# Performance work log

Measured on AMD Instinct MI355X. Metric: run time of the kernel, lower is better.

## Reference

```python
import jax, jax.numpy as jnp
import numpy as np


def setup_inputs() -> dict:
    key = jax.random.key(0)
    k1, k2 = jax.random.split(key)
    # NCHW input activations
    x = jax.random.normal(k1, (32, 256, 56, 56), dtype=jnp.float32)
    # OIHW weight; centered small-uniform so sign() is +/-1 with equal probability
    # (torch init is rand()*0.001, all-positive, which would make sign degenerate
    #  for kernel testing; magnitude scale kept comparable)
    weight = (jax.random.uniform(k2, (256, 256, 3, 3), dtype=jnp.float32) - 0.5) * 0.002
    return {"x": x, "weight": weight}


def reference(x, weight):
    # per-output-channel scaling factor: mean |w| over (in, kh, kw), detached
    scale = jax.lax.stop_gradient(
        jnp.mean(jnp.abs(weight), axis=(1, 2, 3), keepdims=True)
    )  # [O,1,1,1]
    w_clip = jnp.clip(weight, -1.0, 1.0)
    # STE: forward value = scale * sign(w); gradient flows through clip(w)
    binary_w = jax.lax.stop_gradient(scale * jnp.sign(weight) - w_clip) + w_clip
    y = jax.lax.conv_general_dilated(
        x,
        binary_w,
        window_strides=(1, 1),
        padding=((1, 1), (1, 1)),
        dimension_numbers=("NCHW", "OIHW", "NCHW"),
        feature_group_count=1,
    )
    return y
```

## Files before the change

### kernel.cpp

```cpp
#include <hip/hip_runtime.h>
#include <stdint.h>

typedef __attribute__((ext_vector_type(8))) short bf16x8;
typedef __attribute__((ext_vector_type(16))) float f32x16;

#define N_IMG 32
#define CI 256
#define CO 256
#define HH_ 56
#define WW_ 56
#define HP 58
#define WP 58
#define SPP (HP*WP)
#define SPI (HH_*WW_)

#define XB_BYTES ((size_t)N_IMG*SPP*CI*2)
#define W2_OFF   XB_BYTES
#define W2_BYTES ((size_t)9*CO*CI*2)
#define SCALE_OFF (W2_OFF + W2_BYTES)

#define KCP 40

__device__ __forceinline__ unsigned int pack_bf16(float a, float b) {
  unsigned int u0 = __builtin_bit_cast(unsigned int, a);
  unsigned int u1 = __builtin_bit_cast(unsigned int, b);
  u0 = (u0 + 0x7fffu + ((u0 >> 16) & 1u)) >> 16;
  u1 = (u1 + 0x7fffu + ((u1 >> 16) & 1u)) >> 16;
  return u0 | (u1 << 16);
}

__global__ __launch_bounds__(256) void border_zero_k(unsigned short* __restrict__ xb) {
  int gid = blockIdx.x*256 + threadIdx.x;
  int cell = gid >> 5, part = gid & 31;
  int n = cell / 228, b = cell - n*228;
  int h, w;
  if (b < 58)       { h = 0;          w = b;        }
  else if (b < 116) { h = 57;         w = b - 58;   }
  else if (b < 172) { h = b - 116 + 1; w = 0;       }
  else              { h = b - 172 + 1; w = 57;      }
  uint4 z = make_uint4(0u,0u,0u,0u);
  *(uint4*)&xb[((size_t)n*SPP + (size_t)h*WP + w)*CI + part*8] = z;
}

__global__ __launch_bounds__(256) void nchw2nhwc_k(const float* __restrict__ x,
                                                   unsigned short* __restrict__ xb) {
  __shared__ float tile[64*64];
  int bid = blockIdx.x;
  int n = bid / 196; int r = bid - n*196;
  int cb = r / 49;   int t0 = (r - cb*49) * 64;
  int t = threadIdx.x;
  int row = t >> 4, l16 = t & 15;
  const float* src = x + ((size_t)(n*CI + cb*64))*SPI + t0;
#pragma unroll
  for (int it = 0; it < 4; ++it) {
    int c = it*16 + row;
    float4 v = *(const float4*)&src[(size_t)c*SPI + l16*4];
    const float* vf = (const float*)&v;
#pragma unroll
    for (int j = 0; j < 4; ++j) {
      int sp = l16*4 + j;
      int cs = c ^ (((sp >> 2) & 7) << 3);
      tile[sp*64 + cs] = vf[j];
    }
  }
  __syncthreads();
#pragma unroll
  for (int it = 0; it < 2; ++it) {
    int u = it*256 + t;
    int sp = u >> 3, part = u & 7;
    int g = (part*8) ^ (((sp >> 2) & 7) << 3);
    float4 f0 = *(const float4*)&tile[sp*64 + g];
    float4 f1 = *(const float4*)&tile[sp*64 + g + 4];
    const float* a0 = (const float*)&f0; const float* a1 = (const float*)&f1;
    uint4 pk;
    pk.x = pack_bf16(a0[0], a0[1]);
    pk.y = pack_bf16(a0[2], a0[3]);
    pk.z = pack_bf16(a1[0], a1[1]);
    pk.w = pack_bf16(a1[2], a1[3]);
    int spg = t0 + sp; int h = spg / 56; int w = spg - h*56;
    size_t psp = (size_t)(h+1)*WP + (w+1);
    *(uint4*)&xb[((size_t)n*SPP + psp)*CI + cb*64 + part*8] = pk;
  }
}

__global__ __launch_bounds__(256) void prep_w_k(const float* __restrict__ wt,
                                                unsigned short* __restrict__ w2,
                                                float* __restrict__ scale) {
  int o = blockIdx.x; int t = threadIdx.x;
  const float* wr = wt + (size_t)o*2304 + t*9;
  int cc = t >> 5, ks = (t >> 4) & 1, chi = t & 15;
  float s = 0.f;
#pragma unroll
  for (int tap = 0; tap < 9; ++tap) {
    float v = wr[tap];
    s += fabsf(v);
    unsigned short sg = (v > 0.f) ? (unsigned short)0x3F80u
                       : ((v < 0.f) ? (unsigned short)0xBF80u : (unsigned short)0u);
    w2[(size_t)(tap*16 + cc*2 + ks)*4096 + o*16 + chi] = sg;
  }
  __shared__ float red[4];
#pragma unroll
  for (int off = 32; off > 0; off >>= 1) s += __shfl_down(s, off, 64);
  if ((t & 63) == 0) red[t >> 6] = s;
  __syncthreads();
  if (t == 0) scale[o] = (red[0]+red[1]+red[2]+red[3]) * (1.0f/2304.0f);
}

__global__ __launch_bounds__(256, 2) void binconv_k(
    const unsigned short* __restrict__ xb,
    const unsigned short* __restrict__ w2,
    const float* __restrict__ scale,
    float* __restrict__ out) {
  __shared__ unsigned short sp_buf[2][300*KCP];

  int bid = blockIdx.x;
  int orig = (bid & 7)*112 + (bid >> 3);
  int ot = orig & 1, pt = orig >> 1;
  int n = pt / 14, rem = pt - n*14;
  int ht = rem >> 1, wtl = rem & 1;
  int h0 = ht*8, w0 = wtl*28, OB = ot*128;
  int tid = threadIdx.x;
  int lane = tid & 63, wid = tid >> 6;
  int l31 = lane & 31, hi = lane >> 5;

  int pb[7];
#pragma unroll
  for (int f = 0; f < 7; ++f) {
    int px = f*32 + l31;
    int th = px / 28; int tw = px - th*28;
    pb[f] = (th*30 + tw)*KCP + hi*8;
  }

  const unsigned short* wA = w2 + (size_t)(OB + wid*32)*16 + (l31*16 + hi*8);

  const unsigned short* xsrc = xb + ((size_t)n*SPP + (size_t)h0*WP + w0)*CI;

  int goff[5], loff[5]; bool sact[5];
#pragma unroll
  for (int rdi = 0; rdi < 5; ++rdi) {
    int u = rdi*256 + tid;
    sact[rdi] = (u < 1200);
    int px = u >> 2, g = u & 3;
    int hh = px / 30, ww = px - hh*30;
    goff[rdi] = (hh*WP + ww)*CI + g*8;
    loff[rdi] = px*KCP + g*8;
  }

  f32x16 acc[7];
#pragma unroll
  for (int f = 0; f < 7; ++f)
#pragma unroll
    for (int r = 0; r < 16; ++r) acc[f][r] = 0.f;

  uint4 st[5];
#pragma unroll
  for (int rdi = 0; rdi < 5; ++rdi)
    if (sact[rdi]) st[rdi] = *(const uint4*)&xsrc[goff[rdi]];
#pragma unroll
  for (int rdi = 0; rdi < 5; ++rdi)
    if (sact[rdi]) *(uint4*)&sp_buf[0][loff[rdi]] = st[rdi];
  __syncthreads();

  int cur = 0;
  for (int cc = 0; cc < 8; ++cc) {
    if (cc < 7) {
#pragma unroll
      for (int rdi = 0; rdi < 5; ++rdi)
        if (sact[rdi]) st[rdi] = *(const uint4*)&xsrc[goff[rdi] + (cc+1)*32];
    }
    const unsigned short* aCC = wA + (size_t)(cc*2)*4096;
    const unsigned short* sbuf = sp_buf[cur];
#pragma unroll
    for (int tap = 0; tap < 9; ++tap) {
      const int dh = tap / 3, dw = tap - dh*3;
      const int toff = (dh*30 + dw)*KCP;
#pragma unroll
      for (int ks = 0; ks < 2; ++ks) {
        bf16x8 a = *(const bf16x8*)(aCC + (size_t)(tap*16 + ks)*4096);
        bf16x8 bv[7];
#pragma unroll
        for (int f = 0; f < 7; ++f)
          bv[f] = *(const bf16x8*)&sbuf[pb[f] + toff + ks*16];
#pragma unroll
        for (int f = 0; f < 7; ++f)
          acc[f] = __builtin_amdgcn_mfma_f32_32x32x16_bf16(a, bv[f], acc[f], 0, 0, 0);
      }
    }
    if (cc < 7) {
#pragma unroll
      for (int rdi = 0; rdi < 5; ++rdi)
        if (sact[rdi]) *(uint4*)&sp_buf[cur ^ 1][loff[rdi]] = st[rdi];
      __syncthreads();
      cur ^= 1;
    }
  }

  float sc_[16];
#pragma unroll
  for (int r = 0; r < 16; ++r)
    sc_[r] = scale[OB + wid*32 + (r & 3) + 8*(r >> 2) + 4*hi];

#pragma unroll
  for (int f = 0; f < 7; ++f) {
    int px = f*32 + l31;
    int th = px / 28; int tw = px - th*28;
    size_t spo = (size_t)(h0+th)*WW_ + (w0+tw);
#pragma unroll
    for (int r = 0; r < 16; ++r) {
      int o = OB + wid*32 + (r & 3) + 8*(r >> 2) + 4*hi;
      out[((size_t)n*CO + o)*SPI + spo] = acc[f][r] * sc_[r];
    }
  }
}

extern "C" void kernel_launch(void* const* d_in, const int* in_sizes, int n_in,
                              void* d_out, int out_size, void* d_ws, size_t ws_size,
                              hipStream_t stream) {
  const float* x  = (const float*)d_in[0];
  const float* wt = (const float*)d_in[1];
  float* out = (float*)d_out;
  unsigned short* xb = (unsigned short*)d_ws;
  unsigned short* w2 = (unsigned short*)((char*)d_ws + W2_OFF);
  float* scale = (float*)((char*)d_ws + SCALE_OFF);

  border_zero_k<<<912, 256, 0, stream>>>(xb);
  nchw2nhwc_k<<<6272, 256, 0, stream>>>(x, xb);
  prep_w_k<<<256, 256, 0, stream>>>(wt, w2, scale);
  binconv_k<<<896, 256, 0, stream>>>(xb, w2, scale, out);
}
```

Baseline: 363.5 us.

## Fuse prep kernels and restructure binconv with async global-to-LDS pipelining

Merges the border-zero, NCHW-to-NHWC and weight-prep kernels into one launch to cut launch overhead. The conv kernel now uses 512-thread blocks covering full 56-wide rows with 8 waves split over output channels and pixel halves. Weights are staged in LDS through a 4-deep ring and activations are double-buffered, both loaded with async global_load_lds. Activation reads use an XOR swizzle to avoid bank conflicts. This adds per-tap barriers and hand-tuned vmcnt waits, which risks stalls or ordering bugs, and halves the grid to 448 blocks.

```diff
diff --git a/kernel.cpp b/kernel.cpp
--- a/kernel.cpp
+++ b/kernel.cpp
@@ -16,10 +16,10 @@
 
 #define XB_BYTES ((size_t)N_IMG*SPP*CI*2)
 #define W2_OFF   XB_BYTES
-#define W2_BYTES ((size_t)9*CO*CI*2)
-#define SCALE_OFF (W2_OFF + W2_BYTES)
-
-#define KCP 40
+#define SCALE_OFF (W2_OFF + (size_t)9*CO*CI*2)
+
+#define P_UNITS 2320
+#define P_ALLOC 2560
 
 __device__ __forceinline__ unsigned int pack_bf16(float a, float b) {
   unsigned int u0 = __builtin_bit_cast(unsigned int, a);
@@ -29,121 +29,170 @@
   return u0 | (u1 << 16);
 }
 
-__global__ __launch_bounds__(256) void border_zero_k(unsigned short* __restrict__ xb) {
-  int gid = blockIdx.x*256 + threadIdx.x;
-  int cell = gid >> 5, part = gid & 31;
-  int n = cell / 228, b = cell - n*228;
-  int h, w;
-  if (b < 58)       { h = 0;          w = b;        }
-  else if (b < 116) { h = 57;         w = b - 58;   }
-  else if (b < 172) { h = b - 116 + 1; w = 0;       }
-  else              { h = b - 172 + 1; w = 57;      }
-  uint4 z = make_uint4(0u,0u,0u,0u);
-  *(uint4*)&xb[((size_t)n*SPP + (size_t)h*WP + w)*CI + part*8] = z;
-}
-
-__global__ __launch_bounds__(256) void nchw2nhwc_k(const float* __restrict__ x,
-                                                   unsigned short* __restrict__ xb) {
+__device__ __forceinline__ void gl_lds16(const void* g, void* l) {
+  __builtin_amdgcn_global_load_lds(
+      (const __attribute__((address_space(1))) unsigned int*)g,
+      (__attribute__((address_space(3))) unsigned int*)l, 16, 0, 0);
+}
+
+__global__ __launch_bounds__(256) void prep_all_k(const float* __restrict__ x,
+                                                  const float* __restrict__ wt,
+                                                  unsigned short* __restrict__ xb,
+                                                  unsigned short* __restrict__ w2,
+                                                  float* __restrict__ scale) {
   __shared__ float tile[64*64];
+  __shared__ float red[4];
   int bid = blockIdx.x;
-  int n = bid / 196; int r = bid - n*196;
-  int cb = r / 49;   int t0 = (r - cb*49) * 64;
   int t = threadIdx.x;
-  int row = t >> 4, l16 = t & 15;
-  const float* src = x + ((size_t)(n*CI + cb*64))*SPI + t0;
-#pragma unroll
-  for (int it = 0; it < 4; ++it) {
-    int c = it*16 + row;
-    float4 v = *(const float4*)&src[(size_t)c*SPI + l16*4];
-    const float* vf = (const float*)&v;
-#pragma unroll
-    for (int j = 0; j < 4; ++j) {
-      int sp = l16*4 + j;
-      int cs = c ^ (((sp >> 2) & 7) << 3);
-      tile[sp*64 + cs] = vf[j];
-    }
-  }
-  __syncthreads();
-#pragma unroll
-  for (int it = 0; it < 2; ++it) {
-    int u = it*256 + t;
-    int sp = u >> 3, part = u & 7;
-    int g = (part*8) ^ (((sp >> 2) & 7) << 3);
-    float4 f0 = *(const float4*)&tile[sp*64 + g];
-    float4 f1 = *(const float4*)&tile[sp*64 + g + 4];
-    const float* a0 = (const float*)&f0; const float* a1 = (const float*)&f1;
-    uint4 pk;
-    pk.x = pack_bf16(a0[0], a0[1]);
-    pk.y = pack_bf16(a0[2], a0[3]);
-    pk.z = pack_bf16(a1[0], a1[1]);
-    pk.w = pack_bf16(a1[2], a1[3]);
-    int spg = t0 + sp; int h = spg / 56; int w = spg - h*56;
-    size_t psp = (size_t)(h+1)*WP + (w+1);
-    *(uint4*)&xb[((size_t)n*SPP + psp)*CI + cb*64 + part*8] = pk;
-  }
-}
-
-__global__ __launch_bounds__(256) void prep_w_k(const float* __restrict__ wt,
-                                                unsigned short* __restrict__ w2,
-                                                float* __restrict__ scale) {
-  int o = blockIdx.x; int t = threadIdx.x;
-  const float* wr = wt + (size_t)o*2304 + t*9;
-  int cc = t >> 5, ks = (t >> 4) & 1, chi = t & 15;
-  float s = 0.f;
-#pragma unroll
-  for (int tap = 0; tap < 9; ++tap) {
-    float v = wr[tap];
-    s += fabsf(v);
-    unsigned short sg = (v > 0.f) ? (unsigned short)0x3F80u
-                       : ((v < 0.f) ? (unsigned short)0xBF80u : (unsigned short)0u);
-    w2[(size_t)(tap*16 + cc*2 + ks)*4096 + o*16 + chi] = sg;
-  }
-  __shared__ float red[4];
-#pragma unroll
-  for (int off = 32; off > 0; off >>= 1) s += __shfl_down(s, off, 64);
-  if ((t & 63) == 0) red[t >> 6] = s;
-  __syncthreads();
-  if (t == 0) scale[o] = (red[0]+red[1]+red[2]+red[3]) * (1.0f/2304.0f);
-}
-
-__global__ __launch_bounds__(256, 2) void binconv_k(
+  if (bid < 6272) {
+    if (t < 38) {
+      int bu = bid*38 + t;
+      if (bu < 233472) {
+        int cell = bu >> 5, part = bu & 31;
+        int n = cell / 228, b = cell - n*228;
+        int h, w;
+        if (b < 58)       { h = 0;           w = b;       }
+        else if (b < 116) { h = 57;          w = b - 58;  }
+        else if (b < 172) { h = b - 116 + 1; w = 0;       }
+        else              { h = b - 172 + 1; w = 57;      }
+        *(uint4*)&xb[((size_t)n*SPP + (size_t)h*WP + w)*CI + part*8] =
+            make_uint4(0u,0u,0u,0u);
+      }
+    }
+    int n = bid / 196; int r = bid - n*196;
+    int cb = r / 49;   int t0 = (r - cb*49) * 64;
+    int row = t >> 4, l16 = t & 15;
+    const float* src = x + ((size_t)(n*CI + cb*64))*SPI + t0;
+#pragma unroll
+    for (int it = 0; it < 4; ++it) {
+      int c = it*16 + row;
+      float4 v = *(const float4*)&src[(size_t)c*SPI + l16*4];
+      const float* vf = (const float*)&v;
+#pragma unroll
+      for (int j = 0; j < 4; ++j) {
+        int sp = l16*4 + j;
+        int cs = c ^ (((sp >> 2) & 7) << 3);
+        tile[sp*64 + cs] = vf[j];
+      }
+    }
+    __syncthreads();
+#pragma unroll
+    for (int it = 0; it < 2; ++it) {
+      int u = it*256 + t;
+      int sp = u >> 3, part = u & 7;
+      int g = (part*8) ^ (((sp >> 2) & 7) << 3);
+      float4 f0 = *(const float4*)&tile[sp*64 + g];
+      float4 f1 = *(const float4*)&tile[sp*64 + g + 4];
+      const float* a0 = (const float*)&f0; const float* a1 = (const float*)&f1;
+      uint4 pk;
+      pk.x = pack_bf16(a0[0], a0[1]);
+      pk.y = pack_bf16(a0[2], a0[3]);
+      pk.z = pack_bf16(a1[0], a1[1]);
+      pk.w = pack_bf16(a1[2], a1[3]);
+      int spg = t0 + sp; int h = spg / 56; int w = spg - h*56;
+      size_t psp = (size_t)(h+1)*WP + (w+1);
+      *(uint4*)&xb[((size_t)n*SPP + psp)*CI + cb*64 + part*8] = pk;
+    }
+  } else {
+    int o = bid - 6272;
+    const float* wr = wt + (size_t)o*2304 + t*9;
+    int cc = t >> 5, ks = (t >> 4) & 1, hi = (t >> 3) & 1, ch = t & 7;
+    float s = 0.f;
+#pragma unroll
+    for (int tap = 0; tap < 9; ++tap) {
+      float v = wr[tap];
+      s += fabsf(v);
+      unsigned short sg = (v > 0.f) ? (unsigned short)0x3F80u
+                         : ((v < 0.f) ? (unsigned short)0xBF80u : (unsigned short)0u);
+      size_t g = (size_t)(cc*9 + tap);
+      w2[g*8192 + (size_t)(ks*2 + hi)*2048 + (size_t)o*8 + ch] = sg;
+    }
+#pragma unroll
+    for (int off = 32; off > 0; off >>= 1) s += __shfl_down(s, off, 64);
+    if ((t & 63) == 0) red[t >> 6] = s;
+    __syncthreads();
+    if (t == 0) scale[o] = (red[0]+red[1]+red[2]+red[3]) * (1.0f/2304.0f);
+  }
+}
+
+#define TAPB(T, VN, TROW4)                                                      \
+  {                                                                             \
+    int g2 = cc*9 + (T) + 2;                                                    \
+    int gm = (g2 >= 72) ? (g2 - 72) : g2;                                       \
+    gl_lds16(w2 + (size_t)gm*8192 + aSrc, &s_a[((g2 & 3) << 12) + aDst]);       \
+    if ((T) == 0) {                                                             \
+      const unsigned short* ps = xsrc + (cc + 1)*32;                            \
+      _Pragma("unroll")                                                         \
+      for (int k = 0; k < 5; ++k)                                               \
+        gl_lds16(ps + goffP[k], &pn[(k*512 + wbase)*8]);                        \
+    }                                                                           \
+    asm volatile("s_waitcnt vmcnt(" #VN ")" ::: "memory");                      \
+    __builtin_amdgcn_s_barrier();                                               \
+    __builtin_amdgcn_sched_barrier(0);                                          \
+    {                                                                           \
+      const int sb = ((cc + (T)) & 3) << 12;                                    \
+      _Pragma("unroll")                                                         \
+      for (int ks = 0; ks < 2; ++ks) {                                          \
+        bf16x8 a = *(const bf16x8*)&s_a[sb + ks*2048 + aRd];                    \
+        bf16x8 bv[7];                                                           \
+        _Pragma("unroll")                                                       \
+        for (int f = 0; f < 7; ++f) {                                           \
+          int v = ub[f] + (TROW4) + ks*2;                                       \
+          int ph = v ^ ((v >> 3) & 7);                                          \
+          bv[f] = *(const bf16x8*)&sp[ph*8];                                    \
+        }                                                                       \
+        _Pragma("unroll")                                                       \
+        for (int f = 0; f < 7; ++f)                                             \
+          acc[f] = __builtin_amdgcn_mfma_f32_32x32x16_bf16(a, bv[f], acc[f],    \
+                                                           0, 0, 0);            \
+      }                                                                         \
+    }                                                                           \
+  }
+
+__global__ __launch_bounds__(512, 2) void binconv_k(
     const unsigned short* __restrict__ xb,
     const unsigned short* __restrict__ w2,
     const float* __restrict__ scale,
     float* __restrict__ out) {
-  __shared__ unsigned short sp_buf[2][300*KCP];
+  __shared__ unsigned short s_p[2][P_ALLOC*8];
+  __shared__ unsigned short s_a[4*4096];
 
   int bid = blockIdx.x;
-  int orig = (bid & 7)*112 + (bid >> 3);
+  int orig = (bid & 7)*56 + (bid >> 3);
   int ot = orig & 1, pt = orig >> 1;
-  int n = pt / 14, rem = pt - n*14;
-  int ht = rem >> 1, wtl = rem & 1;
-  int h0 = ht*8, w0 = wtl*28, OB = ot*128;
+  int n = pt / 7, ht = pt - n*7;
+  int h0 = ht*8, OB = ot*128;
+
   int tid = threadIdx.x;
   int lane = tid & 63, wid = tid >> 6;
-  int l31 = lane & 31, hi = lane >> 5;
-
-  int pb[7];
+  int l31 = lane & 31, hi_l = lane >> 5;
+  int wo = wid >> 1, wp = wid & 1;
+  int wbase = tid & ~63;
+
+  const int aSrc = ((tid >> 7)*2048) + (OB + (tid & 127))*8;
+  const int aDst = wbase*8;
+  const int aRd = hi_l*1024 + (wo*32 + l31)*8;
+
+  const unsigned short* xsrc = xb + ((size_t)n*SPP + (size_t)h0*WP)*CI;
+
+  int goffP[5];
+#pragma unroll
+  for (int k = 0; k < 5; ++k) {
+    int u = k*512 + tid;
+    int ue = (u > P_UNITS-1) ? (P_UNITS-1) : u;
+    int su = ue ^ ((ue >> 3) & 7);
+    int r = su >> 2, cu = su & 3;
+    int rh = r / 58, rw = r - rh*58;
+    goffP[k] = (rh*WP + rw)*CI + cu*8;
+  }
+
+  int ub[7];
 #pragma unroll
   for (int f = 0; f < 7; ++f) {
-    int px = f*32 + l31;
-    int th = px / 28; int tw = px - th*28;
-    pb[f] = (th*30 + tw)*KCP + hi*8;
-  }
-
-  const unsigned short* wA = w2 + (size_t)(OB + wid*32)*16 + (l31*16 + hi*8);
-
-  const unsigned short* xsrc = xb + ((size_t)n*SPP + (size_t)h0*WP + w0)*CI;
-
-  int goff[5], loff[5]; bool sact[5];
-#pragma unroll
-  for (int rdi = 0; rdi < 5; ++rdi) {
-    int u = rdi*256 + tid;
-    sact[rdi] = (u < 1200);
-    int px = u >> 2, g = u & 3;
-    int hh = px / 30, ww = px - hh*30;
-    goff[rdi] = (hh*WP + ww)*CI + g*8;
-    loff[rdi] = px*KCP + g*8;
+    int idx = f*32 + l31;
+    int hh = wp*4 + idx/56;
+    int ww = idx % 56;
+    ub[f] = (hh*58 + ww)*4 + hi_l;
   }
 
   f32x16 acc[7];
@@ -152,62 +201,44 @@
 #pragma unroll
     for (int r = 0; r < 16; ++r) acc[f][r] = 0.f;
 
-  uint4 st[5];
-#pragma unroll
-  for (int rdi = 0; rdi < 5; ++rdi)
-    if (sact[rdi]) st[rdi] = *(const uint4*)&xsrc[goff[rdi]];
-#pragma unroll
-  for (int rdi = 0; rdi < 5; ++rdi)
-    if (sact[rdi]) *(uint4*)&sp_buf[0][loff[rdi]] = st[rdi];
-  __syncthreads();
-
-  int cur = 0;
+  {
+#pragma unroll
+    for (int k = 0; k < 5; ++k)
+      gl_lds16(xsrc + goffP[k], &s_p[0][(k*512 + wbase)*8]);
+    gl_lds16(w2 + aSrc,                 &s_a[aDst]);
+    gl_lds16(w2 + (size_t)8192 + aSrc,  &s_a[4096 + aDst]);
+  }
+
   for (int cc = 0; cc < 8; ++cc) {
-    if (cc < 7) {
-#pragma unroll
-      for (int rdi = 0; rdi < 5; ++rdi)
-        if (sact[rdi]) st[rdi] = *(const uint4*)&xsrc[goff[rdi] + (cc+1)*32];
-    }
-    const unsigned short* aCC = wA + (size_t)(cc*2)*4096;
-    const unsigned short* sbuf = sp_buf[cur];
-#pragma unroll
-    for (int tap = 0; tap < 9; ++tap) {
-      const int dh = tap / 3, dw = tap - dh*3;
-      const int toff = (dh*30 + dw)*KCP;
-#pragma unroll
-      for (int ks = 0; ks < 2; ++ks) {
-        bf16x8 a = *(const bf16x8*)(aCC + (size_t)(tap*16 + ks)*4096);
-        bf16x8 bv[7];
-#pragma unroll
-        for (int f = 0; f < 7; ++f)
-          bv[f] = *(const bf16x8*)&sbuf[pb[f] + toff + ks*16];
-#pragma unroll
-        for (int f = 0; f < 7; ++f)
-          acc[f] = __builtin_amdgcn_mfma_f32_32x32x16_bf16(a, bv[f], acc[f], 0, 0, 0);
-      }
-    }
-    if (cc < 7) {
-#pragma unroll
-      for (int rdi = 0; rdi < 5; ++rdi)
-        if (sact[rdi]) *(uint4*)&sp_buf[cur ^ 1][loff[rdi]] = st[rdi];
-      __syncthreads();
-      cur ^= 1;
-    }
+    const unsigned short* sp = s_p[cc & 1];
+    unsigned short* pn = s_p[(cc & 1) ^ 1];
+    TAPB(0, 7, 0)
+    TAPB(1, 7, 4)
+    TAPB(2, 7, 8)
+    TAPB(3, 2, 232)
+    TAPB(4, 2, 236)
+    TAPB(5, 2, 240)
+    TAPB(6, 2, 464)
+    TAPB(7, 2, 468)
+    TAPB(8, 2, 472)
+    __builtin_amdgcn_s_barrier();
+    __builtin_amdgcn_sched_barrier(0);
   }
 
   float sc_[16];
 #pragma unroll
   for (int r = 0; r < 16; ++r)
-    sc_[r] = scale[OB + wid*32 + (r & 3) + 8*(r >> 2) + 4*hi];
+    sc_[r] = scale[OB + wo*32 + (r & 3) + 8*(r >> 2) + 4*hi_l];
 
 #pragma unroll
   for (int f = 0; f < 7; ++f) {
-    int px = f*32 + l31;
-    int th = px / 28; int tw = px - th*28;
-    size_t spo = (size_t)(h0+th)*WW_ + (w0+tw);
+    int idx = f*32 + l31;
+    int hh = wp*4 + idx/56;
+    int ww = idx % 56;
+    size_t spo = (size_t)(h0 + hh)*WW_ + ww;
 #pragma unroll
     for (int r = 0; r < 16; ++r) {
-      int o = OB + wid*32 + (r & 3) + 8*(r >> 2) + 4*hi;
+      int o = OB + wo*32 + (r & 3) + 8*(r >> 2) + 4*hi_l;
       out[((size_t)n*CO + o)*SPI + spo] = acc[f][r] * sc_[r];
     }
   }
@@ -223,8 +254,6 @@
   unsigned short* w2 = (unsigned short*)((char*)d_ws + W2_OFF);
   float* scale = (float*)((char*)d_ws + SCALE_OFF);
 
-  border_zero_k<<<912, 256, 0, stream>>>(xb);
-  nchw2nhwc_k<<<6272, 256, 0, stream>>>(x, xb);
-  prep_w_k<<<256, 256, 0, stream>>>(wt, w2, scale);
-  binconv_k<<<896, 256, 0, stream>>>(xb, w2, scale, out);
-}
+  prep_all_k<<<6528, 256, 0, stream>>>(x, wt, xb, w2, scale);
+  binconv_k<<<448, 512, 0, stream>>>(xb, w2, scale, out);
+}
```

Result: faster. 325.8 us (-10.4%).
